# Kernel optimization log

Hardware: AMD Instinct MI355X
Metric: run time of the kernel (lower is better)

The kernel has to match this reference:

```python
import jax, jax.numpy as jnp
import numpy as np

N_NODES = 40000
FEAT = 128
HID = 128
EMB = 64
N_EDGES = 640000


def setup_inputs() -> dict:
    key = jax.random.key(0)
    ks = jax.random.split(key, 8)
    x = jax.random.normal(ks[0], (N_NODES, FEAT), dtype=jnp.float32)
    edge_index = jax.random.randint(ks[1], (2, N_EDGES), 0, N_NODES, dtype=jnp.int64)
    s1 = 1.0 / np.sqrt(FEAT)
    s2 = 1.0 / np.sqrt(HID)
    W1_l = jax.random.uniform(ks[2], (HID, FEAT), jnp.float32, -s1, s1)
    b1 = jax.random.uniform(ks[3], (HID,), jnp.float32, -s1, s1)
    W1_r = jax.random.uniform(ks[4], (HID, FEAT), jnp.float32, -s1, s1)
    W2_l = jax.random.uniform(ks[5], (EMB, HID), jnp.float32, -s2, s2)
    b2 = jax.random.uniform(ks[6], (EMB,), jnp.float32, -s2, s2)
    W2_r = jax.random.uniform(ks[7], (EMB, HID), jnp.float32, -s2, s2)
    return {"x": x, "edge_index": edge_index, "W1_l": W1_l, "b1": b1,
            "W1_r": W1_r, "W2_l": W2_l, "b2": b2, "W2_r": W2_r}


def _sage_conv(x, src, dst, W_l, b_l, W_r, n_nodes):
    # mean aggregation of source-node features onto destination nodes
    msg = x[src]                                           # [E, d]
    agg = jax.ops.segment_sum(msg, dst, num_segments=n_nodes)   # [N, d]
    cnt = jax.ops.segment_sum(jnp.ones((src.shape[0],), x.dtype), dst,
                              num_segments=n_nodes)        # [N]
    agg = agg / jnp.maximum(cnt, 1.0)[:, None]
    # out = lin_l(mean_j x_j) + lin_r(x_i); bias lives in lin_l
    return agg @ W_l.T + b_l + x @ W_r.T


def reference(x, edge_index, W1_l, b1, W1_r, W2_l, b2, W2_r):
    src, dst = edge_index[0], edge_index[1]
    n = x.shape[0]
    h = _sage_conv(x, src, dst, W1_l, b1, W1_r, n)
    h = jax.nn.elu(h)
    # dropout p=0.2 is identity in eval mode
    h = _sage_conv(h, src, dst, W2_l, b2, W2_r, n)
    return jax.nn.log_softmax(h, axis=1)
```

## Files before the change

### kernel.cpp

```cpp
#include <hip/hip_runtime.h>
#include <hip/hip_fp16.h>
#include <math.h>

#define N_NODES 40000
#define FEATD 128
#define EMB 64
#define N_EDGES 640000
#define CAP 64

typedef unsigned short u16;
typedef __attribute__((ext_vector_type(8))) unsigned short u16x8;
typedef __attribute__((ext_vector_type(8))) _Float16 f16x8;
typedef __attribute__((ext_vector_type(4))) float f32x4;

__device__ __forceinline__ float h2f(u16 h) {
  __half hh;
  *(u16*)&hh = h;
  return __half2float(hh);
}
__device__ __forceinline__ u16 f2h(float f) {
  __half hh = __float2half(f);
  return *(u16*)&hh;
}

#define FILL_BLKS 313
#define X_BLKS 1250
#define W_BLKS 192
__global__ __launch_bounds__(256) void prep_fill_kernel(
    const float* __restrict__ x, const float* __restrict__ W1l,
    const float* __restrict__ W1r, const float* __restrict__ W2l,
    const float* __restrict__ W2r, const int* __restrict__ src,
    const int* __restrict__ dst, u16* __restrict__ xh,
    u16* __restrict__ wp, int* __restrict__ deg, u16* __restrict__ bucket) {
  int bid = blockIdx.x;
  if (bid < FILL_BLKS) {
    int t = bid * 256 + threadIdx.x;
    if (t >= N_EDGES / 8) return;
    int4 sa = *(const int4*)(&src[t * 8]);
    int4 sb = *(const int4*)(&src[t * 8 + 4]);
    int4 da = *(const int4*)(&dst[t * 8]);
    int4 db = *(const int4*)(&dst[t * 8 + 4]);
    int p0 = atomicAdd(&deg[da.x], 1);
    int p1 = atomicAdd(&deg[da.y], 1);
    int p2 = atomicAdd(&deg[da.z], 1);
    int p3 = atomicAdd(&deg[da.w], 1);
    int p4 = atomicAdd(&deg[db.x], 1);
    int p5 = atomicAdd(&deg[db.y], 1);
    int p6 = atomicAdd(&deg[db.z], 1);
    int p7 = atomicAdd(&deg[db.w], 1);
    if (p0 < CAP) bucket[da.x * CAP + p0] = (u16)sa.x;
    if (p1 < CAP) bucket[da.y * CAP + p1] = (u16)sa.y;
    if (p2 < CAP) bucket[da.z * CAP + p2] = (u16)sa.z;
    if (p3 < CAP) bucket[da.w * CAP + p3] = (u16)sa.w;
    if (p4 < CAP) bucket[db.x * CAP + p4] = (u16)sb.x;
    if (p5 < CAP) bucket[db.y * CAP + p5] = (u16)sb.y;
    if (p6 < CAP) bucket[db.z * CAP + p6] = (u16)sb.z;
    if (p7 < CAP) bucket[db.w * CAP + p7] = (u16)sb.w;
  } else if (bid < FILL_BLKS + X_BLKS) {
    int i = (bid - FILL_BLKS) * 256 + threadIdx.x;
    float4 v0 = *(const float4*)(&x[i * 16]);
    float4 v1 = *(const float4*)(&x[i * 16 + 4]);
    float4 v2 = *(const float4*)(&x[i * 16 + 8]);
    float4 v3 = *(const float4*)(&x[i * 16 + 12]);
    u16x8 oa, ob;
    oa[0] = f2h(v0.x); oa[1] = f2h(v0.y); oa[2] = f2h(v0.z); oa[3] = f2h(v0.w);
    oa[4] = f2h(v1.x); oa[5] = f2h(v1.y); oa[6] = f2h(v1.z); oa[7] = f2h(v1.w);
    ob[0] = f2h(v2.x); ob[1] = f2h(v2.y); ob[2] = f2h(v2.z); ob[3] = f2h(v2.w);
    ob[4] = f2h(v3.x); ob[5] = f2h(v3.y); ob[6] = f2h(v3.z); ob[7] = f2h(v3.w);
    *(u16x8*)(&xh[i * 16]) = oa;
    *(u16x8*)(&xh[i * 16 + 8]) = ob;
  } else {
    int i = (bid - FILL_BLKS - X_BLKS) * 256 + threadIdx.x;
    const float* srcp;
    int off;
    if (i < 16384)      { srcp = W1l; off = i; }
    else if (i < 32768) { srcp = W1r; off = i - 16384; }
    else if (i < 40960) { srcp = W2l; off = i - 32768; }
    else                { srcp = W2r; off = i - 40960; }
    wp[i] = f2h(srcp[off]);
  }
}

__global__ __launch_bounds__(256) void gather_mean_f16(
    const u16* __restrict__ xh, const int* __restrict__ deg,
    const u16* __restrict__ bucket, u16* __restrict__ aggh) {
  int n = blockIdx.x * 4 + (threadIdx.x >> 6);
  int lane = threadIdx.x & 63;
  int g = lane >> 4;
  int li = lane & 15;
  int dgf = deg[n];
  int dg = dgf < CAP ? dgf : CAP;
  float inv = 1.0f / fmaxf((float)dgf, 1.0f);
  const u16* bk = bucket + n * CAP;
  float a0[8], a1[8], a2[8], a3[8];
#pragma unroll
  for (int i = 0; i < 8; i++) { a0[i] = 0.f; a1[i] = 0.f; a2[i] = 0.f; a3[i] = 0.f; }
  int d = g;
  for (; d + 12 < dg; d += 16) {
    u16x8 v0 = *(const u16x8*)(&xh[(int)bk[d] * 128 + li * 8]);
    u16x8 v1 = *(const u16x8*)(&xh[(int)bk[d + 4] * 128 + li * 8]);
    u16x8 v2 = *(const u16x8*)(&xh[(int)bk[d + 8] * 128 + li * 8]);
    u16x8 v3 = *(const u16x8*)(&xh[(int)bk[d + 12] * 128 + li * 8]);
#pragma unroll
    for (int i = 0; i < 8; i++) {
      a0[i] += h2f(v0[i]); a1[i] += h2f(v1[i]);
      a2[i] += h2f(v2[i]); a3[i] += h2f(v3[i]);
    }
  }
  for (; d < dg; d += 4) {
    u16x8 v0 = *(const u16x8*)(&xh[(int)bk[d] * 128 + li * 8]);
#pragma unroll
    for (int i = 0; i < 8; i++) a0[i] += h2f(v0[i]);
  }
#pragma unroll
  for (int i = 0; i < 8; i++) {
    a0[i] += a1[i] + a2[i] + a3[i];
    a0[i] += __shfl_xor(a0[i], 16);
    a0[i] += __shfl_xor(a0[i], 32);
  }
  if (g == 0) {
    u16x8 o;
#pragma unroll
    for (int i = 0; i < 8; i++) o[i] = f2h(a0[i] * inv);
    *(u16x8*)(&aggh[n * 128 + li * 8]) = o;
  }
}

__global__ __launch_bounds__(256) void gemm12_kernel(
    const u16* __restrict__ AggH, const u16* __restrict__ XH,
    const u16* __restrict__ wp, const float* __restrict__ b1v,
    const float* __restrict__ b2v, u16* __restrict__ Yh,
    float* __restrict__ Z) {
  const u16* w1l = wp;
  const u16* w1r = wp + 16384;
  const u16* w2l = wp + 32768;
  const u16* w2r = wp + 40960;

  __shared__ __align__(16) union {
    struct {
      u16 wl[128][72], wr[128][72];
      u16 a[64][72], x[64][72];
    } p1;
    struct {
      u16 h[64][136];
      u16 w2l[64][136], w2r[64][136];
    } p2;
  } L;

  const int tid = threadIdx.x;
  const int wv = tid >> 6;
  const int lane = tid & 63;
  const int li = lane & 15;
  const int q = lane >> 4;
  const int nbase = blockIdx.x * 64;

  f32x4 acc1[8];
#pragma unroll
  for (int jt = 0; jt < 8; jt++) acc1[jt] = (f32x4){0.f, 0.f, 0.f, 0.f};

  for (int kb = 0; kb < 2; kb++) {
#pragma unroll
    for (int it = 0; it < 4; it++) {
      int idx = tid + 256 * it;
      int j = idx >> 3, c = idx & 7;
      int go = j * 128 + kb * 64 + c * 8;
      *(u16x8*)(&L.p1.wl[j][c * 8]) = *(const u16x8*)(&w1l[go]);
      *(u16x8*)(&L.p1.wr[j][c * 8]) = *(const u16x8*)(&w1r[go]);
    }
#pragma unroll
    for (int it = 0; it < 2; it++) {
      int idx = tid + 256 * it;
      int n = idx >> 3, c = idx & 7;
      int go = (nbase + n) * 128 + kb * 64 + c * 8;
      *(u16x8*)(&L.p1.a[n][c * 8]) = *(const u16x8*)(&AggH[go]);
      *(u16x8*)(&L.p1.x[n][c * 8]) = *(const u16x8*)(&XH[go]);
    }
    __syncthreads();
#pragma unroll
    for (int kk = 0; kk < 2; kk++) {
      f16x8 aF = *(const f16x8*)(&L.p1.a[wv * 16 + li][kk * 32 + q * 8]);
      f16x8 xF = *(const f16x8*)(&L.p1.x[wv * 16 + li][kk * 32 + q * 8]);
#pragma unroll
      for (int jt = 0; jt < 8; jt++) {
        f16x8 wlF = *(const f16x8*)(&L.p1.wl[jt * 16 + li][kk * 32 + q * 8]);
        f16x8 wrF = *(const f16x8*)(&L.p1.wr[jt * 16 + li][kk * 32 + q * 8]);
        acc1[jt] = __builtin_amdgcn_mfma_f32_16x16x32_f16(aF, wlF, acc1[jt], 0, 0, 0);
        acc1[jt] = __builtin_amdgcn_mfma_f32_16x16x32_f16(xF, wrF, acc1[jt], 0, 0, 0);
      }
    }
    __syncthreads();
  }

#pragma unroll
  for (int jt = 0; jt < 8; jt++) {
    int j = jt * 16 + li;
    float bb = b1v[j];
#pragma unroll
    for (int r = 0; r < 4; r++) {
      float v = acc1[jt][r] + bb;
      v = v > 0.f ? v : expm1f(v);
      L.p2.h[wv * 16 + q * 4 + r][j] = f2h(v);
    }
  }
#pragma unroll
  for (int it = 0; it < 4; it++) {
    int idx = tid + 256 * it;
    int j = idx >> 4, c = idx & 15;
    int go = j * 128 + c * 8;
    *(u16x8*)(&L.p2.w2l[j][c * 8]) = *(const u16x8*)(&w2l[go]);
    *(u16x8*)(&L.p2.w2r[j][c * 8]) = *(const u16x8*)(&w2r[go]);
  }
  __syncthreads();

  f32x4 accY[4], accZ[4];
#pragma unroll
  for (int mt = 0; mt < 4; mt++) {
    accY[mt] = (f32x4){0.f, 0.f, 0.f, 0.f};
    accZ[mt] = (f32x4){0.f, 0.f, 0.f, 0.f};
  }
#pragma unroll
  for (int kc = 0; kc < 4; kc++) {
    f16x8 blF = *(const f16x8*)(&L.p2.w2l[wv * 16 + li][kc * 32 + q * 8]);
    f16x8 brF = *(const f16x8*)(&L.p2.w2r[wv * 16 + li][kc * 32 + q * 8]);
#pragma unroll
    for (int mt = 0; mt < 4; mt++) {
      f16x8 hF = *(const f16x8*)(&L.p2.h[mt * 16 + li][kc * 32 + q * 8]);
      accY[mt] = __builtin_amdgcn_mfma_f32_16x16x32_f16(hF, blF, accY[mt], 0, 0, 0);
      accZ[mt] = __builtin_amdgcn_mfma_f32_16x16x32_f16(hF, brF, accZ[mt], 0, 0, 0);
    }
  }

  {
    int j2 = wv * 16 + li;
    float bb = b2v[j2];
#pragma unroll
    for (int mt = 0; mt < 4; mt++) {
#pragma unroll
      for (int r = 0; r < 4; r++) {
        int node = nbase + mt * 16 + q * 4 + r;
        Yh[node * 64 + j2] = f2h(accY[mt][r]);
        Z[node * 64 + j2] = accZ[mt][r] + bb;
      }
    }
  }
}

__global__ __launch_bounds__(256) void final_kernel(
    const u16* __restrict__ Y, const float* __restrict__ Z,
    const int* __restrict__ deg, const u16* __restrict__ bucket,
    float* __restrict__ out) {
  int n = blockIdx.x * 4 + (threadIdx.x >> 6);
  int lane = threadIdx.x & 63;
  int g = lane >> 4;
  int li = lane & 15;
  int dgf = deg[n];
  int dg = dgf < CAP ? dgf : CAP;
  float inv = 1.0f / fmaxf((float)dgf, 1.0f);
  const u16* bk = bucket + n * CAP;
  float4 a0 = {0.f, 0.f, 0.f, 0.f}, a1 = {0.f, 0.f, 0.f, 0.f};
  float4 a2 = {0.f, 0.f, 0.f, 0.f}, a3 = {0.f, 0.f, 0.f, 0.f};
  int d = g;
  for (; d + 12 < dg; d += 16) {
    ushort4 v0 = *(const ushort4*)(&Y[(int)bk[d] * 64 + li * 4]);
    ushort4 v1 = *(const ushort4*)(&Y[(int)bk[d + 4] * 64 + li * 4]);
    ushort4 v2 = *(const ushort4*)(&Y[(int)bk[d + 8] * 64 + li * 4]);
    ushort4 v3 = *(const ushort4*)(&Y[(int)bk[d + 12] * 64 + li * 4]);
    a0.x += h2f(v0.x); a0.y += h2f(v0.y); a0.z += h2f(v0.z); a0.w += h2f(v0.w);
    a1.x += h2f(v1.x); a1.y += h2f(v1.y); a1.z += h2f(v1.z); a1.w += h2f(v1.w);
    a2.x += h2f(v2.x); a2.y += h2f(v2.y); a2.z += h2f(v2.z); a2.w += h2f(v2.w);
    a3.x += h2f(v3.x); a3.y += h2f(v3.y); a3.z += h2f(v3.z); a3.w += h2f(v3.w);
  }
  for (; d < dg; d += 4) {
    ushort4 v0 = *(const ushort4*)(&Y[(int)bk[d] * 64 + li * 4]);
    a0.x += h2f(v0.x); a0.y += h2f(v0.y); a0.z += h2f(v0.z); a0.w += h2f(v0.w);
  }
  a0.x += a1.x + a2.x + a3.x; a0.y += a1.y + a2.y + a3.y;
  a0.z += a1.z + a2.z + a3.z; a0.w += a1.w + a2.w + a3.w;
  a0.x += __shfl_xor(a0.x, 16); a0.y += __shfl_xor(a0.y, 16);
  a0.z += __shfl_xor(a0.z, 16); a0.w += __shfl_xor(a0.w, 16);
  a0.x += __shfl_xor(a0.x, 32); a0.y += __shfl_xor(a0.y, 32);
  a0.z += __shfl_xor(a0.z, 32); a0.w += __shfl_xor(a0.w, 32);
  float4 zb = *(const float4*)(&Z[n * 64 + li * 4]);
  float4 v;
  v.x = zb.x + a0.x * inv; v.y = zb.y + a0.y * inv;
  v.z = zb.z + a0.z * inv; v.w = zb.w + a0.w * inv;
  float m = fmaxf(fmaxf(v.x, v.y), fmaxf(v.z, v.w));
  m = fmaxf(m, __shfl_xor(m, 1)); m = fmaxf(m, __shfl_xor(m, 2));
  m = fmaxf(m, __shfl_xor(m, 4)); m = fmaxf(m, __shfl_xor(m, 8));
  float s = __expf(v.x - m) + __expf(v.y - m) + __expf(v.z - m) + __expf(v.w - m);
  s += __shfl_xor(s, 1); s += __shfl_xor(s, 2);
  s += __shfl_xor(s, 4); s += __shfl_xor(s, 8);
  float lg = m + logf(s);
  if (lane < 16) {
    float4 o = {v.x - lg, v.y - lg, v.z - lg, v.w - lg};
    *(float4*)(&out[n * 64 + li * 4]) = o;
  }
}

extern "C" void kernel_launch(void* const* d_in, const int* in_sizes, int n_in,
                              void* d_out, int out_size, void* d_ws, size_t ws_size,
                              hipStream_t stream) {
  const float* x   = (const float*)d_in[0];
  const int*   ei  = (const int*)d_in[1];
  const float* W1l = (const float*)d_in[2];
  const float* b1  = (const float*)d_in[3];
  const float* W1r = (const float*)d_in[4];
  const float* W2l = (const float*)d_in[5];
  const float* b2  = (const float*)d_in[6];
  const float* W2r = (const float*)d_in[7];
  float* out = (float*)d_out;

  const int* src = ei;
  const int* dst = ei + N_EDGES;

  u16* bucket = (u16*)d_ws;
  int* deg = (int*)(bucket + (size_t)N_NODES * CAP);
  u16* xh = (u16*)(deg + N_NODES);
  u16* aggh = xh + (size_t)N_NODES * FEATD;
  u16* yh = aggh + (size_t)N_NODES * FEATD;
  float* z = (float*)(yh + (size_t)N_NODES * EMB);
  u16* wp = (u16*)(z + (size_t)N_NODES * EMB);

  hipMemsetAsync(deg, 0, N_NODES * sizeof(int), stream);
  prep_fill_kernel<<<FILL_BLKS + X_BLKS + W_BLKS, 256, 0, stream>>>(
      x, W1l, W1r, W2l, W2r, src, dst, xh, wp, deg, bucket);
  gather_mean_f16<<<N_NODES / 4, 256, 0, stream>>>(xh, deg, bucket, aggh);
  gemm12_kernel<<<N_NODES / 64, 256, 0, stream>>>(aggh, xh, wp, b1, b2, yh, z);
  final_kernel<<<N_NODES / 4, 256, 0, stream>>>(yh, z, deg, bucket, out);
}
```

Measured before the change: 186.7 us.

## Fuse layer-1 neighbor gather into GEMM kernel and store Z in fp16

Moves the mean-aggregation gather for layer 1 into the GEMM kernel: each block gathers neighbor features for its 64 nodes into shared memory, then runs the MFMA GEMMs from there. This drops one kernel launch and the write and re-read of the 40000x128 fp16 aggregate buffer. The Z output is also stored as fp16 instead of fp32, halving that traffic. The trade-off is far fewer parallel waves for the latency-bound gather (625 blocks instead of 10000), larger LDS use that may lower occupancy, and reduced precision in Z.

```diff
diff --git a/kernel.cpp b/kernel.cpp
--- a/kernel.cpp
+++ b/kernel.cpp
@@ -81,56 +81,11 @@
   }
 }
 
-__global__ __launch_bounds__(256) void gather_mean_f16(
-    const u16* __restrict__ xh, const int* __restrict__ deg,
-    const u16* __restrict__ bucket, u16* __restrict__ aggh) {
-  int n = blockIdx.x * 4 + (threadIdx.x >> 6);
-  int lane = threadIdx.x & 63;
-  int g = lane >> 4;
-  int li = lane & 15;
-  int dgf = deg[n];
-  int dg = dgf < CAP ? dgf : CAP;
-  float inv = 1.0f / fmaxf((float)dgf, 1.0f);
-  const u16* bk = bucket + n * CAP;
-  float a0[8], a1[8], a2[8], a3[8];
-#pragma unroll
-  for (int i = 0; i < 8; i++) { a0[i] = 0.f; a1[i] = 0.f; a2[i] = 0.f; a3[i] = 0.f; }
-  int d = g;
-  for (; d + 12 < dg; d += 16) {
-    u16x8 v0 = *(const u16x8*)(&xh[(int)bk[d] * 128 + li * 8]);
-    u16x8 v1 = *(const u16x8*)(&xh[(int)bk[d + 4] * 128 + li * 8]);
-    u16x8 v2 = *(const u16x8*)(&xh[(int)bk[d + 8] * 128 + li * 8]);
-    u16x8 v3 = *(const u16x8*)(&xh[(int)bk[d + 12] * 128 + li * 8]);
-#pragma unroll
-    for (int i = 0; i < 8; i++) {
-      a0[i] += h2f(v0[i]); a1[i] += h2f(v1[i]);
-      a2[i] += h2f(v2[i]); a3[i] += h2f(v3[i]);
-    }
-  }
-  for (; d < dg; d += 4) {
-    u16x8 v0 = *(const u16x8*)(&xh[(int)bk[d] * 128 + li * 8]);
-#pragma unroll
-    for (int i = 0; i < 8; i++) a0[i] += h2f(v0[i]);
-  }
-#pragma unroll
-  for (int i = 0; i < 8; i++) {
-    a0[i] += a1[i] + a2[i] + a3[i];
-    a0[i] += __shfl_xor(a0[i], 16);
-    a0[i] += __shfl_xor(a0[i], 32);
-  }
-  if (g == 0) {
-    u16x8 o;
-#pragma unroll
-    for (int i = 0; i < 8; i++) o[i] = f2h(a0[i] * inv);
-    *(u16x8*)(&aggh[n * 128 + li * 8]) = o;
-  }
-}
-
 __global__ __launch_bounds__(256) void gemm12_kernel(
-    const u16* __restrict__ AggH, const u16* __restrict__ XH,
-    const u16* __restrict__ wp, const float* __restrict__ b1v,
-    const float* __restrict__ b2v, u16* __restrict__ Yh,
-    float* __restrict__ Z) {
+    const u16* __restrict__ xh, const u16* __restrict__ wp,
+    const float* __restrict__ b1v, const float* __restrict__ b2v,
+    const int* __restrict__ deg, const u16* __restrict__ bucket,
+    u16* __restrict__ Yh, u16* __restrict__ Zh) {
   const u16* w1l = wp;
   const u16* w1r = wp + 16384;
   const u16* w2l = wp + 32768;
@@ -139,7 +94,8 @@
   __shared__ __align__(16) union {
     struct {
       u16 wl[128][72], wr[128][72];
-      u16 a[64][72], x[64][72];
+      u16 x[64][72];
+      u16 agg[64][136];
     } p1;
     struct {
       u16 h[64][136];
@@ -154,6 +110,48 @@
   const int q = lane >> 4;
   const int nbase = blockIdx.x * 64;
 
+  for (int it = 0; it < 16; it++) {
+    int nl = wv * 16 + it;
+    int gn = nbase + nl;
+    int dgf = deg[gn];
+    int dg = dgf < CAP ? dgf : CAP;
+    float inv = 1.0f / fmaxf((float)dgf, 1.0f);
+    const u16* bk = bucket + (size_t)gn * CAP;
+    float a0[8], a1[8], a2[8], a3[8];
+#pragma unroll
+    for (int i = 0; i < 8; i++) { a0[i] = 0.f; a1[i] = 0.f; a2[i] = 0.f; a3[i] = 0.f; }
+    int d = q;
+    for (; d + 12 < dg; d += 16) {
+      u16x8 v0 = *(const u16x8*)(&xh[(int)bk[d] * 128 + li * 8]);
+      u16x8 v1 = *(const u16x8*)(&xh[(int)bk[d + 4] * 128 + li * 8]);
+      u16x8 v2 = *(const u16x8*)(&xh[(int)bk[d + 8] * 128 + li * 8]);
+      u16x8 v3 = *(const u16x8*)(&xh[(int)bk[d + 12] * 128 + li * 8]);
+#pragma unroll
+      for (int i = 0; i < 8; i++) {
+        a0[i] += h2f(v0[i]); a1[i] += h2f(v1[i]);
+        a2[i] += h2f(v2[i]); a3[i] += h2f(v3[i]);
+      }
+    }
+    for (; d < dg; d += 4) {
+      u16x8 v0 = *(const u16x8*)(&xh[(int)bk[d] * 128 + li * 8]);
+#pragma unroll
+      for (int i = 0; i < 8; i++) a0[i] += h2f(v0[i]);
+    }
+#pragma unroll
+    for (int i = 0; i < 8; i++) {
+      a0[i] += a1[i] + a2[i] + a3[i];
+      a0[i] += __shfl_xor(a0[i], 16);
+      a0[i] += __shfl_xor(a0[i], 32);
+    }
+    if (q == 0) {
+      u16x8 o;
+#pragma unroll
+      for (int i = 0; i < 8; i++) o[i] = f2h(a0[i] * inv);
+      *(u16x8*)(&L.p1.agg[nl][li * 8]) = o;
+    }
+  }
+  __syncthreads();
+
   f32x4 acc1[8];
 #pragma unroll
   for (int jt = 0; jt < 8; jt++) acc1[jt] = (f32x4){0.f, 0.f, 0.f, 0.f};
@@ -172,13 +170,12 @@
       int idx = tid + 256 * it;
       int n = idx >> 3, c = idx & 7;
       int go = (nbase + n) * 128 + kb * 64 + c * 8;
-      *(u16x8*)(&L.p1.a[n][c * 8]) = *(const u16x8*)(&AggH[go]);
-      *(u16x8*)(&L.p1.x[n][c * 8]) = *(const u16x8*)(&XH[go]);
+      *(u16x8*)(&L.p1.x[n][c * 8]) = *(const u16x8*)(&xh[go]);
     }
     __syncthreads();
 #pragma unroll
     for (int kk = 0; kk < 2; kk++) {
-      f16x8 aF = *(const f16x8*)(&L.p1.a[wv * 16 + li][kk * 32 + q * 8]);
+      f16x8 aF = *(const f16x8*)(&L.p1.agg[wv * 16 + li][kb * 64 + kk * 32 + q * 8]);
       f16x8 xF = *(const f16x8*)(&L.p1.x[wv * 16 + li][kk * 32 + q * 8]);
 #pragma unroll
       for (int jt = 0; jt < 8; jt++) {
@@ -239,14 +236,14 @@
       for (int r = 0; r < 4; r++) {
         int node = nbase + mt * 16 + q * 4 + r;
         Yh[node * 64 + j2] = f2h(accY[mt][r]);
-        Z[node * 64 + j2] = accZ[mt][r] + bb;
+        Zh[node * 64 + j2] = f2h(accZ[mt][r] + bb);
       }
     }
   }
 }
 
 __global__ __launch_bounds__(256) void final_kernel(
-    const u16* __restrict__ Y, const float* __restrict__ Z,
+    const u16* __restrict__ Y, const u16* __restrict__ Z,
     const int* __restrict__ deg, const u16* __restrict__ bucket,
     float* __restrict__ out) {
   int n = blockIdx.x * 4 + (threadIdx.x >> 6);
@@ -280,10 +277,10 @@
   a0.z += __shfl_xor(a0.z, 16); a0.w += __shfl_xor(a0.w, 16);
   a0.x += __shfl_xor(a0.x, 32); a0.y += __shfl_xor(a0.y, 32);
   a0.z += __shfl_xor(a0.z, 32); a0.w += __shfl_xor(a0.w, 32);
-  float4 zb = *(const float4*)(&Z[n * 64 + li * 4]);
+  ushort4 zb4 = *(const ushort4*)(&Z[n * 64 + li * 4]);
   float4 v;
-  v.x = zb.x + a0.x * inv; v.y = zb.y + a0.y * inv;
-  v.z = zb.z + a0.z * inv; v.w = zb.w + a0.w * inv;
+  v.x = h2f(zb4.x) + a0.x * inv; v.y = h2f(zb4.y) + a0.y * inv;
+  v.z = h2f(zb4.z) + a0.z * inv; v.w = h2f(zb4.w) + a0.w * inv;
   float m = fmaxf(fmaxf(v.x, v.y), fmaxf(v.z, v.w));
   m = fmaxf(m, __shfl_xor(m, 1)); m = fmaxf(m, __shfl_xor(m, 2));
   m = fmaxf(m, __shfl_xor(m, 4)); m = fmaxf(m, __shfl_xor(m, 8));
@@ -316,15 +313,13 @@
   u16* bucket = (u16*)d_ws;
   int* deg = (int*)(bucket + (size_t)N_NODES * CAP);
   u16* xh = (u16*)(deg + N_NODES);
-  u16* aggh = xh + (size_t)N_NODES * FEATD;
-  u16* yh = aggh + (size_t)N_NODES * FEATD;
-  float* z = (float*)(yh + (size_t)N_NODES * EMB);
-  u16* wp = (u16*)(z + (size_t)N_NODES * EMB);
+  u16* yh = xh + (size_t)N_NODES * FEATD;
+  u16* zh = yh + (size_t)N_NODES * EMB;
+  u16* wp = zh + (size_t)N_NODES * EMB;
 
   hipMemsetAsync(deg, 0, N_NODES * sizeof(int), stream);
   prep_fill_kernel<<<FILL_BLKS + X_BLKS + W_BLKS, 256, 0, stream>>>(
       x, W1l, W1r, W2l, W2r, src, dst, xh, wp, deg, bucket);
-  gather_mean_f16<<<N_NODES / 4, 256, 0, stream>>>(xh, deg, bucket, aggh);
-  gemm12_kernel<<<N_NODES / 64, 256, 0, stream>>>(aggh, xh, wp, b1, b2, yh, z);
-  final_kernel<<<N_NODES / 4, 256, 0, stream>>>(yh, z, deg, bucket, out);
-}
+  gemm12_kernel<<<N_NODES / 64, 256, 0, stream>>>(xh, wp, b1, b2, deg, bucket, yh, zh);
+  final_kernel<<<N_NODES / 4, 256, 0, stream>>>(yh, zh, deg, bucket, out);
+}
```

After: 230.0 us. 1.23x slower.
